# Kernel tuning notes

Measured on AMD Instinct MI355X. Metric: run time of the kernel, lower is better.

## Reference

```python
import jax, jax.numpy as jnp
import numpy as np

B, P, K = 32, 2048, 20   # events, points per event, kNN neighbors
EPS = 1e-5               # BatchNorm eps (eval mode, running stats)


def setup_inputs() -> dict:
    key = jax.random.key(0)
    ks = iter(jax.random.split(key, 64))
    inp = {}
    inp["x"] = jax.random.normal(next(ks), (B * P, 7), jnp.float32)
    inp["batch"] = jnp.repeat(jnp.arange(B, dtype=jnp.int32), P)

    def add_layer(tag, cin, cout):
        inp["w" + tag] = jax.random.normal(next(ks), (cin, cout), jnp.float32) / np.sqrt(cin)
        inp["b" + tag] = jax.random.normal(next(ks), (cout,), jnp.float32) * 0.01
        inp["g" + tag] = jax.random.uniform(next(ks), (cout,), jnp.float32, 0.5, 1.5)
        inp["e" + tag] = jax.random.normal(next(ks), (cout,), jnp.float32) * 0.1
        inp["m" + tag] = jax.random.normal(next(ks), (cout,), jnp.float32) * 0.1
        inp["v" + tag] = jax.random.uniform(next(ks), (cout,), jnp.float32, 0.5, 1.5)

    # conv1 MLP: [14, 64, 64, 64]
    add_layer("10", 14, 64)
    add_layer("11", 64, 64)
    add_layer("12", 64, 64)
    # conv2 MLP: [128, 128]
    add_layer("20", 128, 128)
    return inp


def _lin_relu_bn(h, W, b, g, be, rm, rv):
    # Linear -> ReLU -> BatchNorm1d (eval mode: running stats)
    h = jax.nn.relu(h @ W + b)
    return (h - rm) * (g / jnp.sqrt(rv + EPS)) + be


def _knn_idx(x):
    # x: [B, P, C] -> indices of K nearest neighbors (incl. self), [B, P, K]
    sq = jnp.sum(x * x, axis=-1)                                   # [B, P]
    d = sq[:, :, None] + sq[:, None, :] - 2.0 * jnp.einsum("bpc,bqc->bpq", x, x)
    _, idx = jax.lax.top_k(-d, K)
    return idx


def _edge_conv(x, mlp):
    # DynamicEdgeConv: kNN graph on current features, edge MLP([x_i, x_j - x_i]), max-aggr
    idx = _knn_idx(x)                                              # [B, P, K]
    xj = jax.vmap(lambda xb, ib: xb[ib])(x, idx)                   # [B, P, K, C]
    xi = jnp.broadcast_to(x[:, :, None, :], xj.shape)
    e = jnp.concatenate([xi, xj - xi], axis=-1)                    # [B, P, K, 2C]
    return jnp.max(mlp(e), axis=2)                                 # [B, P, Cout]


def reference(x, batch,
              w10, b10, g10, e10, m10, v10,
              w11, b11, g11, e11, m11, v11,
              w12, b12, g12, e12, m12, v12,
              w20, b20, g20, e20, m20, v20):
    xb = x.reshape(B, P, -1)                                       # fixed-size events

    def mlp1(e):
        h = _lin_relu_bn(e, w10, b10, g10, e10, m10, v10)
        h = _lin_relu_bn(h, w11, b11, g11, e11, m11, v11)
        return _lin_relu_bn(h, w12, b12, g12, e12, m12, v12)

    def mlp2(e):
        return _lin_relu_bn(e, w20, b20, g20, e20, m20, v20)

    x1 = _edge_conv(xb, mlp1)                                      # [B, P, 64]
    x2 = _edge_conv(x1, mlp2)                                      # [B, P, 128]
    out = jnp.concatenate([x1, x2], axis=-1).reshape(B * P, 192)
    return out, batch
```

## Files before the change

kernel.cpp:

```cpp
#include <hip/hip_runtime.h>

#define B_EV 32
#define P_PT 2048
#define K_NN 20
#define NPTS (B_EV*P_PT)
#define EPS_BN 1e-5f
#define RINF 3.0e38f

typedef _Float16 half8 __attribute__((ext_vector_type(8)));
typedef float f32x4 __attribute__((ext_vector_type(4)));

static constexpr int oWA10=0, oWB10=448, oB10=896, oT10=960,
  oT11=5184,
  oT12=9408,
  oWA20=9472, oWB20=17664, oB20=25856, oT20=25984,
  oB11p=26048, oB12p=26112,
  oW11hi=26176, oW11lo=28224,
  oW12hi=30272, oW12lo=32320;
static constexpr size_t oIDX = 36864;
static constexpr size_t oA1  = 1347584;
static constexpr size_t oB1  = oA1 + (size_t)NPTS*64;
static constexpr size_t oV2  = oB1 + (size_t)NPTS*64;
static constexpr size_t oX1  = oV2 + (size_t)NPTS*128;
static constexpr size_t oSQ  = oX1 + (size_t)NPTS*64;
static constexpr size_t oD   = oSQ + (size_t)NPTS;
static constexpr size_t oU2  = oA1;

__global__ __launch_bounds__(128) void k_prep(
  const float* w10,const float* b10,const float* g10,const float* e10,const float* m10,const float* v10,
  const float* w11,const float* b11,const float* g11,const float* e11,const float* m11,const float* v11,
  const float* w12,const float* b12,const float* g12,const float* e12,const float* m12,const float* v12,
  const float* w20,const float* b20,const float* g20,const float* e20,const float* m20,const float* v20,
  float* ws)
{
  __shared__ float t10s[64], t11s[64];
  int c = threadIdx.x;
  if (c < 64) {
    float s0 = g10[c]*rsqrtf(v10[c]+EPS_BN);
    ws[oB10+c]=b10[c]*s0;
    float t10 = e10[c]-m10[c]*s0; ws[oT10+c]=t10; t10s[c]=t10;
    for (int i=0;i<7;i++){
      ws[oWA10+i*64+c]=(w10[i*64+c]-w10[(7+i)*64+c])*s0;
      ws[oWB10+i*64+c]=w10[(7+i)*64+c]*s0;
    }
    float s1 = g11[c]*rsqrtf(v11[c]+EPS_BN);
    float t11 = e11[c]-m11[c]*s1; ws[oT11+c]=t11; t11s[c]=t11;
    float s2 = g12[c]*rsqrtf(v12[c]+EPS_BN);
    ws[oT12+c]=e12[c]-m12[c]*s2;
  }
  __syncthreads();
  if (c < 64) {
    float s1 = g11[c]*rsqrtf(v11[c]+EPS_BN);
    _Float16* W1hi = (_Float16*)(ws + oW11hi);
    _Float16* W1lo = (_Float16*)(ws + oW11lo);
    float acc = b11[c]*s1;
    for (int i=0;i<64;i++){
      float wv = w11[i*64+c]*s1;
      _Float16 h = (_Float16)wv;
      W1hi[c*64+i] = h;
      W1lo[c*64+i] = (_Float16)(wv - (float)h);
      acc = fmaf(t10s[i], wv, acc);
    }
    ws[oB11p+c]=acc;
    float s2 = g12[c]*rsqrtf(v12[c]+EPS_BN);
    _Float16* W2hi = (_Float16*)(ws + oW12hi);
    _Float16* W2lo = (_Float16*)(ws + oW12lo);
    float acc2 = b12[c]*s2;
    for (int i=0;i<64;i++){
      float wv = w12[i*64+c]*s2;
      _Float16 h = (_Float16)wv;
      W2hi[c*64+i] = h;
      W2lo[c*64+i] = (_Float16)(wv - (float)h);
      acc2 = fmaf(t11s[i], wv, acc2);
    }
    ws[oB12p+c]=acc2;
  }
  {
    float s = g20[c]*rsqrtf(v20[c]+EPS_BN);
    ws[oB20+c]=b20[c]*s; ws[oT20+c]=e20[c]-m20[c]*s;
    for (int i=0;i<64;i++){
      ws[oWA20+i*128+c]=(w20[i*128+c]-w20[(64+i)*128+c])*s;
      ws[oWB20+i*128+c]=w20[(64+i)*128+c]*s;
    }
  }
}

__device__ __forceinline__ void select20(float (&d)[32], int lane, int base, int g,
                                         int* __restrict__ idxout)
{
  float g4[4];
  #pragma unroll
  for (int k=0;k<4;k++){
    float m = d[8*k];
    #pragma unroll
    for (int j=1;j<8;j++) m = fminf(m, d[8*k+j]);
    g4[k]=m;
  }
  float T = 0.f;
  #pragma unroll 1
  for (int pass=0; pass<20; ++pass){
    float m = fminf(fminf(g4[0],g4[1]), fminf(g4[2],g4[3]));
    #pragma unroll
    for (int off=32; off>0; off>>=1) m = fminf(m, __shfl_xor(m, off, 64));
    if (pass==19){ T=m; break; }
    #pragma unroll
    for (int k=0;k<4;k++){
      if (g4[k]==m){
        #pragma unroll
        for (int j=0;j<8;j++) d[8*k+j] = (d[8*k+j]==m) ? RINF : d[8*k+j];
        float mm = d[8*k];
        #pragma unroll
        for (int j=1;j<8;j++) mm = fminf(mm, d[8*k+j]);
        g4[k]=mm;
      }
    }
  }
  int cnt=0;
  #pragma unroll
  for (int j=0;j<32;j++){
    bool take = (d[j]>=RINF) || (d[j]==T);
    unsigned long long mb = __ballot(take);
    if (take){
      int pos = cnt + (int)__popcll(mb & ((1ull<<lane)-1ull));
      if (pos < K_NN) idxout[(size_t)g*K_NN + pos] = base + j*64 + lane;
    }
    cnt += (int)__popcll(mb);
  }
  if (lane==0){
    for (int r=cnt; r<K_NN; ++r) idxout[(size_t)g*K_NN + r] = g;
  }
}

__global__ __launch_bounds__(512) void k_knn1(const float* __restrict__ x, int* __restrict__ idxout)
{
  __shared__ float xs[P_PT*7];
  int t = threadIdx.x;
  int b = blockIdx.x;
  int xcd = b & 7, kk = b >> 3;
  int e = xcd + ((kk >> 8) << 3);
  int blk = kk & 255;
  const float4* src = (const float4*)(x + (size_t)e*P_PT*7);
  #pragma unroll
  for (int u=0;u<7;u++) ((float4*)xs)[u*512+t] = src[u*512+t];
  __syncthreads();
  int lane = t & 63;
  int g = e*P_PT + blk*8 + (t>>6);
  int pin = g & (P_PT-1);
  float xp[7];
  #pragma unroll
  for (int i=0;i<7;i++) xp[i]=xs[pin*7+i];
  float d[32];
  #pragma unroll
  for (int j=0;j<32;j++){
    const float* xq = xs + (j*64+lane)*7;
    float s=0.f;
    #pragma unroll
    for (int i=0;i<7;i++){ float df=xp[i]-xq[i]; s=fmaf(df,df,s); }
    d[j]=s;
  }
  select20(d, lane, e*P_PT, g, idxout);
}

__global__ __launch_bounds__(256) void k_ab1(const float* __restrict__ x, const float* __restrict__ W,
                                             float* __restrict__ A1, float* __restrict__ B1)
{
  int g = blockIdx.x*256+threadIdx.x;
  float xi[7];
  #pragma unroll
  for (int i=0;i<7;i++) xi[i]=x[(size_t)g*7+i];
  float a[64], b[64];
  #pragma unroll
  for (int c=0;c<64;c++){ a[c]=W[oB10+c]; b[c]=0.f; }
  #pragma unroll
  for (int i=0;i<7;i++){
    #pragma unroll
    for (int c=0;c<64;c++) a[c]=fmaf(xi[i], W[oWA10+i*64+c], a[c]);
    #pragma unroll
    for (int c=0;c<64;c++) b[c]=fmaf(xi[i], W[oWB10+i*64+c], b[c]);
  }
  #pragma unroll
  for (int c=0;c<64;c+=4){
    float4 oa; oa.x=a[c]; oa.y=a[c+1]; oa.z=a[c+2]; oa.w=a[c+3];
    *(float4*)(A1+(size_t)g*64+c)=oa;
    float4 ob; ob.x=b[c]; ob.y=b[c+1]; ob.z=b[c+2]; ob.w=b[c+3];
    *(float4*)(B1+(size_t)g*64+c)=ob;
  }
}

__global__ __launch_bounds__(256, 2) void k_ec1m(const int* __restrict__ idx, const float* __restrict__ ws,
    const float* __restrict__ A1, const float* __restrict__ B1,
    float* __restrict__ x1, float* __restrict__ sqv, float* __restrict__ out)
{
  __shared__ float h2s[4][48*64];
  int t = threadIdx.x, w = t>>6, lane = t&63;
  int b = blockIdx.x;
  int xcd = b & 7, kk = b >> 3;
  int ev = xcd + ((kk >> 8) << 3);
  int iA = ev*P_PT + (kk & 255)*8 + w*2;
  int iB = iA + 1;
  int lg = lane>>4, lr = lane&15;

  int jT0 = idx[(size_t)iA*K_NN + lr];
  int jT1 = idx[(size_t)iB*K_NN + lr];
  int a2 = (lr < 4) ? iA*K_NN + 16 + lr : iB*K_NN + 12 + lr;
  a2 = (lr < 8) ? a2 : 0;
  int jT2 = (lr < 8) ? idx[a2] : iA;

  const float* ApA = A1 + (size_t)iA*64;
  const float* ApB = A1 + (size_t)iB*64;
  float4 avA[2][2], avB[2][2], bv[3][2][2];
  const float* Bp0 = B1 + (size_t)jT0*64;
  const float* Bp1 = B1 + (size_t)jT1*64;
  const float* Bp2 = B1 + (size_t)jT2*64;
  #pragma unroll
  for (int ks=0;ks<2;ks++){
    int c0 = ks*32 + lg*8;
    avA[ks][0] = *(const float4*)(ApA+c0); avA[ks][1] = *(const float4*)(ApA+c0+4);
    avB[ks][0] = *(const float4*)(ApB+c0); avB[ks][1] = *(const float4*)(ApB+c0+4);
    bv[0][ks][0] = *(const float4*)(Bp0+c0); bv[0][ks][1] = *(const float4*)(Bp0+c0+4);
    bv[1][ks][0] = *(const float4*)(Bp1+c0); bv[1][ks][1] = *(const float4*)(Bp1+c0+4);
    bv[2][ks][0] = *(const float4*)(Bp2+c0); bv[2][ks][1] = *(const float4*)(Bp2+c0+4);
  }

  bool useB2 = (lr >= 4) && (lr < 8);
  half8 AH[3][2], AL[3][2];
  #pragma unroll
  for (int tile=0;tile<3;tile++){
    #pragma unroll
    for (int ks=0;ks<2;ks++){
      float4 a0, a1;
      if (tile==0){ a0 = avA[ks][0]; a1 = avA[ks][1]; }
      else if (tile==1){ a0 = avB[ks][0]; a1 = avB[ks][1]; }
      else {
        a0.x = useB2 ? avB[ks][0].x : avA[ks][0].x;  a0.y = useB2 ? avB[ks][0].y : avA[ks][0].y;
        a0.z = useB2 ? avB[ks][0].z : avA[ks][0].z;  a0.w = useB2 ? avB[ks][0].w : avA[ks][0].w;
        a1.x = useB2 ? avB[ks][1].x : avA[ks][1].x;  a1.y = useB2 ? avB[ks][1].y : avA[ks][1].y;
        a1.z = useB2 ? avB[ks][1].z : avA[ks][1].z;  a1.w = useB2 ? avB[ks][1].w : avA[ks][1].w;
      }
      float hv[8];
      hv[0]=fmaxf(a0.x+bv[tile][ks][0].x,0.f); hv[1]=fmaxf(a0.y+bv[tile][ks][0].y,0.f);
      hv[2]=fmaxf(a0.z+bv[tile][ks][0].z,0.f); hv[3]=fmaxf(a0.w+bv[tile][ks][0].w,0.f);
      hv[4]=fmaxf(a1.x+bv[tile][ks][1].x,0.f); hv[5]=fmaxf(a1.y+bv[tile][ks][1].y,0.f);
      hv[6]=fmaxf(a1.z+bv[tile][ks][1].z,0.f); hv[7]=fmaxf(a1.w+bv[tile][ks][1].w,0.f);
      half8 ah, al;
      #pragma unroll
      for (int q=0;q<8;q++){
        _Float16 h = (_Float16)hv[q];
        ah[q]=h; al[q]=(_Float16)(hv[q]-(float)h);
      }
      AH[tile][ks]=ah; AL[tile][ks]=al;
    }
  }

  f32x4 acc[3][4];
  #pragma unroll
  for (int nt=0;nt<4;nt++){
    float bb = ws[oB11p + nt*16 + lr];
    f32x4 v = {bb,bb,bb,bb};
    acc[0][nt]=v; acc[1][nt]=v; acc[2][nt]=v;
  }
  {
    const _Float16* W1hi = (const _Float16*)(ws + oW11hi);
    const _Float16* W1lo = (const _Float16*)(ws + oW11lo);
    #pragma unroll
    for (int nt=0;nt<4;nt++){
      const _Float16* whp = W1hi + (nt*16+lr)*64 + lg*8;
      const _Float16* wlp = W1lo + (nt*16+lr)*64 + lg*8;
      half8 wh0 = *(const half8*)(whp);
      half8 wh1 = *(const half8*)(whp+32);
      half8 wl0 = *(const half8*)(wlp);
      half8 wl1 = *(const half8*)(wlp+32);
      #pragma unroll
      for (int tile=0;tile<3;tile++){
        acc[tile][nt] = __builtin_amdgcn_mfma_f32_16x16x32_f16(AH[tile][0], wh0, acc[tile][nt], 0,0,0);
        acc[tile][nt] = __builtin_amdgcn_mfma_f32_16x16x32_f16(AL[tile][0], wh0, acc[tile][nt], 0,0,0);
        acc[tile][nt] = __builtin_amdgcn_mfma_f32_16x16x32_f16(AH[tile][0], wl0, acc[tile][nt], 0,0,0);
        acc[tile][nt] = __builtin_amdgcn_mfma_f32_16x16x32_f16(AH[tile][1], wh1, acc[tile][nt], 0,0,0);
        acc[tile][nt] = __builtin_amdgcn_mfma_f32_16x16x32_f16(AL[tile][1], wh1, acc[tile][nt], 0,0,0);
        acc[tile][nt] = __builtin_amdgcn_mfma_f32_16x16x32_f16(AH[tile][1], wl1, acc[tile][nt], 0,0,0);
      }
    }
  }

  float* hb = h2s[w];
  #pragma unroll
  for (int tile=0;tile<3;tile++){
    #pragma unroll
    for (int nt=0;nt<4;nt++){
      #pragma unroll
      for (int r=0;r<4;r++){
        int row = tile*16 + lg*4 + r;
        int col = nt*16 + lr;
        int baddr = (row*256 + col*4) ^ ((row&7)<<4);
        *(float*)((char*)hb + baddr) = fmaxf(acc[tile][nt][r], 0.f);
      }
    }
  }

  half8 AH2[3][2], AL2[3][2];
  #pragma unroll
  for (int tile=0;tile<3;tile++){
    #pragma unroll
    for (int ks=0;ks<2;ks++){
      int row = tile*16 + lr;
      int byte0 = (row*256 + (ks*32 + lg*8)*4);
      int s = (row&7)<<4;
      f32x4 v0 = *(const f32x4*)((char*)hb + ((byte0)^s));
      f32x4 v1 = *(const f32x4*)((char*)hb + ((byte0+16)^s));
      half8 ah, al;
      #pragma unroll
      for (int q=0;q<4;q++){
        _Float16 h = (_Float16)v0[q];
        ah[q]=h; al[q]=(_Float16)(v0[q]-(float)h);
      }
      #pragma unroll
      for (int q=0;q<4;q++){
        _Float16 h = (_Float16)v1[q];
        ah[4+q]=h; al[4+q]=(_Float16)(v1[q]-(float)h);
      }
      AH2[tile][ks]=ah; AL2[tile][ks]=al;
    }
  }

  f32x4 acc2[3][4];
  #pragma unroll
  for (int nt=0;nt<4;nt++){
    float bb = ws[oB12p + nt*16 + lr];
    f32x4 v = {bb,bb,bb,bb};
    acc2[0][nt]=v; acc2[1][nt]=v; acc2[2][nt]=v;
  }
  {
    const _Float16* W2hi = (const _Float16*)(ws + oW12hi);
    const _Float16* W2lo = (const _Float16*)(ws + oW12lo);
    #pragma unroll
    for (int nt=0;nt<4;nt++){
      const _Float16* whp = W2hi + (nt*16+lr)*64 + lg*8;
      const _Float16* wlp = W2lo + (nt*16+lr)*64 + lg*8;
      half8 wh0 = *(const half8*)(whp);
      half8 wh1 = *(const half8*)(whp+32);
      half8 wl0 = *(const half8*)(wlp);
      half8 wl1 = *(const half8*)(wlp+32);
      #pragma unroll
      for (int tile=0;tile<3;tile++){
        acc2[tile][nt] = __builtin_amdgcn_mfma_f32_16x16x32_f16(AH2[tile][0], wh0, acc2[tile][nt], 0,0,0);
        acc2[tile][nt] = __builtin_amdgcn_mfma_f32_16x16x32_f16(AL2[tile][0], wh0, acc2[tile][nt], 0,0,0);
        acc2[tile][nt] = __builtin_amdgcn_mfma_f32_16x16x32_f16(AH2[tile][0], wl0, acc2[tile][nt], 0,0,0);
        acc2[tile][nt] = __builtin_amdgcn_mfma_f32_16x16x32_f16(AH2[tile][1], wh1, acc2[tile][nt], 0,0,0);
        acc2[tile][nt] = __builtin_amdgcn_mfma_f32_16x16x32_f16(AL2[tile][1], wh1, acc2[tile][nt], 0,0,0);
        acc2[tile][nt] = __builtin_amdgcn_mfma_f32_16x16x32_f16(AH2[tile][1], wl1, acc2[tile][nt], 0,0,0);
      }
    }
  }

  float finA[4], finB[4];
  float sqA = 0.f, sqB = 0.f;
  #pragma unroll
  for (int nt=0;nt<4;nt++){
    float cvA = -RINF;
    #pragma unroll
    for (int r=0;r<4;r++) cvA = fmaxf(cvA, acc2[0][nt][r]);
    if (lg==0){
      #pragma unroll
      for (int r=0;r<4;r++) cvA = fmaxf(cvA, acc2[2][nt][r]);
    }
    cvA = fmaxf(cvA, __shfl_xor(cvA,16,64));
    cvA = fmaxf(cvA, __shfl_xor(cvA,32,64));
    finA[nt] = fmaxf(cvA, 0.f) + ws[oT12 + nt*16 + lr];
    sqA = fmaf(finA[nt], finA[nt], sqA);

    float cvB = -RINF;
    #pragma unroll
    for (int r=0;r<4;r++) cvB = fmaxf(cvB, acc2[1][nt][r]);
    if (lg==1){
      #pragma unroll
      for (int r=0;r<4;r++) cvB = fmaxf(cvB, acc2[2][nt][r]);
    }
    cvB = fmaxf(cvB, __shfl_xor(cvB,16,64));
    cvB = fmaxf(cvB, __shfl_xor(cvB,32,64));
    finB[nt] = fmaxf(cvB, 0.f) + ws[oT12 + nt*16 + lr];
    sqB = fmaf(finB[nt], finB[nt], sqB);
  }
  if (lane < 16){
    #pragma unroll
    for (int nt=0;nt<4;nt++){
      x1[(size_t)iA*64 + nt*16 + lane] = finA[nt];
      out[(size_t)iA*192 + nt*16 + lane] = finA[nt];
      x1[(size_t)iB*64 + nt*16 + lane] = finB[nt];
      out[(size_t)iB*192 + nt*16 + lane] = finB[nt];
    }
  }
  #pragma unroll
  for (int off=1; off<16; off<<=1){
    sqA += __shfl_xor(sqA, off, 64);
    sqB += __shfl_xor(sqB, off, 64);
  }
  if (lane == 0){ sqv[iA] = sqA; sqv[iB] = sqB; }
}

__global__ __launch_bounds__(256) void k_dist2(const float* __restrict__ x1, const float* __restrict__ sqv,
                                               float* __restrict__ D, int e0, int ce)
{
  __shared__ float As[64][68], Bs[64][68];
  int b = blockIdx.x;
  int z, inner;
  if (ce == 8){ z = b & 7; inner = b >> 3; }
  else        { z = b / 1024; inner = b % 1024; }
  int by = inner >> 5, bx = inner & 31;
  int e = e0 + z;
  const float* Xe = x1 + (size_t)e*P_PT*64;
  int rb = by*64, cb = bx*64;
  int t = threadIdx.x;
  int tr = t>>4, tk=(t&15)*4;
  #pragma unroll
  for (int rr=0;rr<4;rr++){
    int r = tr + 16*rr;
    float4 va = *(const float4*)(Xe + (size_t)(rb+r)*64 + tk);
    As[tk][r]=va.x; As[tk+1][r]=va.y; As[tk+2][r]=va.z; As[tk+3][r]=va.w;
    float4 vb = *(const float4*)(Xe + (size_t)(cb+r)*64 + tk);
    Bs[tk][r]=vb.x; Bs[tk+1][r]=vb.y; Bs[tk+2][r]=vb.z; Bs[tk+3][r]=vb.w;
  }
  __syncthreads();
  int tx=t&15, ty=t>>4;
  float acc[4][4];
  #pragma unroll
  for (int i=0;i<4;i++){
    #pragma unroll
    for (int j=0;j<4;j++) acc[i][j]=0.f;
  }
  #pragma unroll 4
  for (int k=0;k<64;k++){
    float4 a4 = *(const float4*)(&As[k][ty*4]);
    float4 b4 = *(const float4*)(&Bs[k][tx*4]);
    float a0=a4.x, a1=a4.y, a2=a4.z, a3=a4.w;
    float b0=b4.x, b1=b4.y, b2=b4.z, b3=b4.w;
    acc[0][0]=fmaf(a0,b0,acc[0][0]); acc[0][1]=fmaf(a0,b1,acc[0][1]);
    acc[0][2]=fmaf(a0,b2,acc[0][2]); acc[0][3]=fmaf(a0,b3,acc[0][3]);
    acc[1][0]=fmaf(a1,b0,acc[1][0]); acc[1][1]=fmaf(a1,b1,acc[1][1]);
    acc[1][2]=fmaf(a1,b2,acc[1][2]); acc[1][3]=fmaf(a1,b3,acc[1][3]);
    acc[2][0]=fmaf(a2,b0,acc[2][0]); acc[2][1]=fmaf(a2,b1,acc[2][1]);
    acc[2][2]=fmaf(a2,b2,acc[2][2]); acc[2][3]=fmaf(a2,b3,acc[2][3]);
    acc[3][0]=fmaf(a3,b0,acc[3][0]); acc[3][1]=fmaf(a3,b1,acc[3][1]);
    acc[3][2]=fmaf(a3,b2,acc[3][2]); acc[3][3]=fmaf(a3,b3,acc[3][3]);
  }
  float sr[4], sc[4];
  #pragma unroll
  for (int i=0;i<4;i++){ sr[i]=sqv[e*P_PT + rb+ty*4+i]; sc[i]=sqv[e*P_PT + cb+tx*4+i]; }
  #pragma unroll
  for (int i=0;i<4;i++){
    float4 o;
    o.x = sr[i]+sc[0]-2.f*acc[i][0];
    o.y = sr[i]+sc[1]-2.f*acc[i][1];
    o.z = sr[i]+sc[2]-2.f*acc[i][2];
    o.w = sr[i]+sc[3]-2.f*acc[i][3];
    *(float4*)(D + (size_t)(z*P_PT + rb+ty*4+i)*P_PT + cb + tx*4) = o;
  }
}

__global__ __launch_bounds__(256) void k_sel2(const float* __restrict__ D, int* __restrict__ idxout, int e0)
{
  int t=threadIdx.x, lane=t&63;
  int pl = blockIdx.x*4 + (t>>6);
  int le = pl>>11, pin = pl&(P_PT-1);
  int e = e0 + le;
  int g = e*P_PT + pin;
  const float* Dr = D + (size_t)pl*P_PT;
  float d[32];
  #pragma unroll
  for (int j=0;j<32;j++) d[j]=Dr[j*64+lane];
  select20(d, lane, e*P_PT, g, idxout);
}

__global__ __launch_bounds__(256) void k_uv2(const float* __restrict__ x1, const float* __restrict__ W,
                                             float* __restrict__ U2, float* __restrict__ V2)
{
  int g = blockIdx.x*256 + threadIdx.x;
  int half = blockIdx.y & 1;
  bool isU = blockIdx.y < 2;
  const float* Wb = W + (isU?oWA20:oWB20) + half*64;
  float acc[64];
  #pragma unroll
  for (int c=0;c<64;c++) acc[c] = isU ? W[oB20+half*64+c] : 0.f;
  const float* xp = x1 + (size_t)g*64;
  #pragma unroll 1
  for (int i=0;i<64;i+=4){
    float4 xv = *(const float4*)(xp+i);
    #pragma unroll
    for (int c=0;c<64;c++) acc[c]=fmaf(xv.x, Wb[(i+0)*128+c], acc[c]);
    #pragma unroll
    for (int c=0;c<64;c++) acc[c]=fmaf(xv.y, Wb[(i+1)*128+c], acc[c]);
    #pragma unroll
    for (int c=0;c<64;c++) acc[c]=fmaf(xv.z, Wb[(i+2)*128+c], acc[c]);
    #pragma unroll
    for (int c=0;c<64;c++) acc[c]=fmaf(xv.w, Wb[(i+3)*128+c], acc[c]);
  }
  float* dst = (isU?U2:V2) + (size_t)g*128 + half*64;
  #pragma unroll
  for (int c=0;c<64;c+=4){
    float4 o; o.x=acc[c]; o.y=acc[c+1]; o.z=acc[c+2]; o.w=acc[c+3];
    *(float4*)(dst+c)=o;
  }
}

__global__ __launch_bounds__(256) void k_gather2(const int* __restrict__ idx, const float* __restrict__ U2,
     const float* __restrict__ V2, const float* __restrict__ W, float* __restrict__ out)
{
  int b = blockIdx.x;
  int xcd = b & 7, kk = b >> 3;
  int ev = xcd + ((kk >> 3) << 3);
  int g = ev*P_PT + (kk & 7)*256 + threadIdx.x;
  int half = blockIdx.y;
  float mx[64];
  #pragma unroll
  for (int c=0;c<64;c++) mx[c]=-RINF;
  for (int k=0;k<K_NN;k++){
    int j = idx[(size_t)g*K_NN+k];
    const float4* vp = (const float4*)(V2 + (size_t)j*128 + half*64);
    #pragma unroll
    for (int c4=0;c4<16;c4++){
      float4 v=vp[c4];
      mx[c4*4+0]=fmaxf(mx[c4*4+0],v.x);
      mx[c4*4+1]=fmaxf(mx[c4*4+1],v.y);
      mx[c4*4+2]=fmaxf(mx[c4*4+2],v.z);
      mx[c4*4+3]=fmaxf(mx[c4*4+3],v.w);
    }
  }
  const float* Up = U2 + (size_t)g*128 + half*64;
  float* op = out + (size_t)g*192 + 64 + half*64;
  #pragma unroll
  for (int c=0;c<64;c+=4){
    float4 o;
    o.x = fmaxf(Up[c+0]+mx[c+0],0.f)+W[oT20+half*64+c+0];
    o.y = fmaxf(Up[c+1]+mx[c+1],0.f)+W[oT20+half*64+c+1];
    o.z = fmaxf(Up[c+2]+mx[c+2],0.f)+W[oT20+half*64+c+2];
    o.w = fmaxf(Up[c+3]+mx[c+3],0.f)+W[oT20+half*64+c+3];
    *(float4*)(op+c)=o;
  }
}

__global__ __launch_bounds__(256) void k_batchf(const int* __restrict__ batch, float* __restrict__ out){
  int i = blockIdx.x*256+threadIdx.x;
  out[(size_t)NPTS*192 + i] = (float)batch[i];
}

extern "C" void kernel_launch(void* const* d_in, const int* in_sizes, int n_in,
                              void* d_out, int out_size, void* d_ws, size_t ws_size,
                              hipStream_t stream)
{
  const float* x     = (const float*)d_in[0];
  const int*   batch = (const int*)d_in[1];
  const float* w10=(const float*)d_in[2],  *b10=(const float*)d_in[3],  *g10=(const float*)d_in[4],
             *e10=(const float*)d_in[5],  *m10=(const float*)d_in[6],  *v10=(const float*)d_in[7];
  const float* w11=(const float*)d_in[8],  *b11=(const float*)d_in[9],  *g11=(const float*)d_in[10],
             *e11=(const float*)d_in[11], *m11=(const float*)d_in[12], *v11=(const float*)d_in[13];
  const float* w12=(const float*)d_in[14], *b12=(const float*)d_in[15], *g12=(const float*)d_in[16],
             *e12=(const float*)d_in[17], *m12=(const float*)d_in[18], *v12=(const float*)d_in[19];
  const float* w20=(const float*)d_in[20], *b20=(const float*)d_in[21], *g20=(const float*)d_in[22],
             *e20=(const float*)d_in[23], *m20=(const float*)d_in[24], *v20=(const float*)d_in[25];

  float* ws  = (float*)d_ws;
  float* out = (float*)d_out;
  int*   idxp = (int*)(ws + oIDX);

  k_prep<<<1,128,0,stream>>>(w10,b10,g10,e10,m10,v10, w11,b11,g11,e11,m11,v11,
                             w12,b12,g12,e12,m12,v12, w20,b20,g20,e20,m20,v20, ws);
  k_knn1<<<NPTS/8, 512, 0, stream>>>(x, idxp);
  k_ab1<<<NPTS/256, 256, 0, stream>>>(x, ws, ws+oA1, ws+oB1);
  k_ec1m<<<NPTS/8, 256, 0, stream>>>(idxp, ws, ws+oA1, ws+oB1, ws+oX1, ws+oSQ, out);

  size_t wsFloats = ws_size/4;
  long avail = (long)wsFloats - (long)oD;
  int CE = (int)(avail / (2048L*2048L));
  if (CE < 1) CE = 1;
  if (CE > 8) CE = 8;
  for (int e0=0; e0<B_EV; e0+=CE){
    int ce = (B_EV - e0 < CE) ? (B_EV - e0) : CE;
    k_dist2<<<ce*1024,256,0,stream>>>(ws+oX1, ws+oSQ, ws+oD, e0, ce);
    k_sel2<<<ce*512,256,0,stream>>>(ws+oD, idxp, e0);
  }

  k_uv2<<<dim3(NPTS/256,4),256,0,stream>>>(ws+oX1, ws, ws+oU2, ws+oV2);
  k_gather2<<<dim3(NPTS/256,2),256,0,stream>>>(idxp, ws+oU2, ws+oV2, ws, out);
  k_batchf<<<NPTS/256,256,0,stream>>>(batch, out);
}
```

Baseline: 1.064 ms.

## Pad kNN1 shared points to 8 floats with XOR swizzle and larger blocks

The first kNN kernel now stores each point as 8 padded floats in LDS using an XOR swizzle, so each candidate point is read with two 128-bit loads instead of seven strided scalar loads. Blocks grow to 1024 threads handling 16 query points each, which halves the number of times each event's point cloud is reloaded into LDS. In exchange, LDS use rises to 64KB per block, and the launch_bounds(1024, 8) hint may constrain register allocation. The global-to-shared copy is now uncoalesced scalar loads instead of float4 loads.

New measurement: 1.002 ms. 5.8% less time.

```diff
diff --git a/kernel.cpp b/kernel.cpp
--- a/kernel.cpp
+++ b/kernel.cpp
@@ -131,31 +131,58 @@
   }
 }
 
-__global__ __launch_bounds__(512) void k_knn1(const float* __restrict__ x, int* __restrict__ idxout)
-{
-  __shared__ float xs[P_PT*7];
+__global__ __launch_bounds__(1024, 8) void k_knn1(const float* __restrict__ x, int* __restrict__ idxout)
+{
+  __shared__ float xs[P_PT*8];
   int t = threadIdx.x;
   int b = blockIdx.x;
   int xcd = b & 7, kk = b >> 3;
-  int e = xcd + ((kk >> 8) << 3);
-  int blk = kk & 255;
-  const float4* src = (const float4*)(x + (size_t)e*P_PT*7);
-  #pragma unroll
-  for (int u=0;u<7;u++) ((float4*)xs)[u*512+t] = src[u*512+t];
+  int e = xcd + ((kk >> 7) << 3);
+  int blk = kk & 127;
+  {
+    const float* xe = x + (size_t)e*P_PT*7;
+    #pragma unroll
+    for (int u=0; u<2; u++){
+      int p = t + u*1024;
+      float v0=xe[p*7+0], v1=xe[p*7+1], v2=xe[p*7+2], v3=xe[p*7+3];
+      float v4=xe[p*7+4], v5=xe[p*7+5], v6=xe[p*7+6];
+      int s = (p&7)<<2;
+      int w0 = (p*8) ^ s;
+      int w1 = (p*8+4) ^ s;
+      f32x4 lo = {v0,v1,v2,v3};
+      f32x4 hi = {v4,v5,v6,0.f};
+      *(f32x4*)(xs + w0) = lo;
+      *(f32x4*)(xs + w1) = hi;
+    }
+  }
   __syncthreads();
   int lane = t & 63;
-  int g = e*P_PT + blk*8 + (t>>6);
+  int g = e*P_PT + blk*16 + (t>>6);
   int pin = g & (P_PT-1);
   float xp[7];
-  #pragma unroll
-  for (int i=0;i<7;i++) xp[i]=xs[pin*7+i];
+  {
+    int s = (pin&7)<<2;
+    f32x4 lo = *(const f32x4*)(xs + ((pin*8)^s));
+    f32x4 hi = *(const f32x4*)(xs + ((pin*8+4)^s));
+    xp[0]=lo[0]; xp[1]=lo[1]; xp[2]=lo[2]; xp[3]=lo[3];
+    xp[4]=hi[0]; xp[5]=hi[1]; xp[6]=hi[2];
+  }
+  int sl = (lane&7)<<2;
+  const float* base0 = xs + ((lane*8)^sl);
+  const float* base1 = xs + ((lane*8+4)^sl);
   float d[32];
   #pragma unroll
   for (int j=0;j<32;j++){
-    const float* xq = xs + (j*64+lane)*7;
-    float s=0.f;
-    #pragma unroll
-    for (int i=0;i<7;i++){ float df=xp[i]-xq[i]; s=fmaf(df,df,s); }
+    f32x4 lo = *(const f32x4*)(base0 + j*512);
+    f32x4 hi = *(const f32x4*)(base1 + j*512);
+    float s=0.f, df;
+    df = xp[0]-lo[0]; s=fmaf(df,df,s);
+    df = xp[1]-lo[1]; s=fmaf(df,df,s);
+    df = xp[2]-lo[2]; s=fmaf(df,df,s);
+    df = xp[3]-lo[3]; s=fmaf(df,df,s);
+    df = xp[4]-hi[0]; s=fmaf(df,df,s);
+    df = xp[5]-hi[1]; s=fmaf(df,df,s);
+    df = xp[6]-hi[2]; s=fmaf(df,df,s);
     d[j]=s;
   }
   select20(d, lane, e*P_PT, g, idxout);
@@ -563,7 +590,7 @@
 
   k_prep<<<1,128,0,stream>>>(w10,b10,g10,e10,m10,v10, w11,b11,g11,e11,m11,v11,
                              w12,b12,g12,e12,m12,v12, w20,b20,g20,e20,m20,v20, ws);
-  k_knn1<<<NPTS/8, 512, 0, stream>>>(x, idxp);
+  k_knn1<<<NPTS/16, 1024, 0, stream>>>(x, idxp);
   k_ab1<<<NPTS/256, 256, 0, stream>>>(x, ws, ws+oA1, ws+oB1);
   k_ec1m<<<NPTS/8, 256, 0, stream>>>(idxp, ws, ws+oA1, ws+oB1, ws+oX1, ws+oSQ, out);
 
```
